# Kernel optimization log

Hardware: AMD Instinct MI355X
Metric: run time of the kernel (lower is better)

## Reference

```python
import jax, jax.numpy as jnp
import numpy as np

H = 64          # hiddens_dims
K = 3           # Chebyshev order
B = 16          # graphs in batch
NPG = 16384     # nodes per graph
N = B * NPG     # total nodes
E = 2_097_152   # total edges
R = 2191        # num_residues (hard-coded in source)
E_REF = R * 16
HALF = N // 2   # backbone count == sidechain count (mask is balanced per graph)


def _lin(k, fan_in, shape):
    return jax.random.uniform(k, shape, jnp.float32, -1.0, 1.0) / np.sqrt(fan_in)


def setup_inputs() -> dict:
    key = jax.random.key(0)
    ks = jax.random.split(key, 40)
    inp = {}
    inp["x"] = jax.random.normal(ks[0], (N, 3), jnp.float32)
    inp["edge_index"] = jax.random.randint(ks[1], (2, E), 0, N)
    inp["batch"] = jnp.repeat(jnp.arange(B, dtype=jnp.int32), NPG)
    blk = jnp.concatenate([jnp.ones((NPG // 2,), bool), jnp.zeros((NPG // 2,), bool)])
    inp["mask"] = jnp.tile(blk, B)  # backbone=True first half of each graph block
    inp["x_ref"] = jax.random.normal(ks[2], (R, 3), jnp.float32)
    inp["edgeref"] = jax.random.randint(ks[3], (2, E_REF), 0, R)
    i = 4
    for name, cin in [("cw0", 3), ("cw1", H), ("cw2", H), ("rw0", 3), ("rw1", H), ("rw2", H)]:
        inp[name] = _lin(ks[i], cin, (K, cin, H)); i += 1
        inp[name.replace("w", "b")] = jnp.zeros((H,), jnp.float32)  # ChebConv bias init = zeros
    for name, cin, cout in [("mlp_w", 2 * H, H), ("mlpP2_w", 2 * H, H),
                            ("rep0_w", H, H), ("rep1_w", H, H), ("rep2_w", H, 3)]:
        inp[name] = _lin(ks[i], cin, (cin, cout)); i += 1
        inp[name.replace("_w", "_b")] = _lin(ks[i], cin, (cout,)); i += 1
    return inp


def cheb_conv(x, edge_index, W, b, n):
    # PyG ChebConv with sym normalization, lambda_max=2: L_hat = -D^-1/2 A D^-1/2 (diag = 0)
    row, col = edge_index[0], edge_index[1]
    deg = jax.ops.segment_sum(jnp.ones_like(x[:, 0])[row] * 0 + 1.0, row, num_segments=n)
    dinv = jnp.where(deg > 0, jax.lax.rsqrt(jnp.maximum(deg, 1e-12)), 0.0)
    w = -(dinv[row] * dinv[col])  # [E]

    def prop(h):  # L_hat @ h via gather + segment_sum
        return jax.ops.segment_sum(w[:, None] * h[col], row, num_segments=n)

    Tx0 = x
    out = Tx0 @ W[0]
    Tx1 = prop(x)
    out = out + Tx1 @ W[1]
    for k in range(2, K):
        Tx2 = 2.0 * prop(Tx1) - Tx0
        out = out + Tx2 @ W[k]
        Tx0, Tx1 = Tx1, Tx2
    return out + b


def _forward(x, edge_index, mask, x_ref, edgeref,
             cw0, cb0, cw1, cb1, cw2, cb2, rw0, rb0, rw1, rb1, rw2, rb2,
             mlp_w, mlp_b, mlpP2_w, mlpP2_b,
             rep0_w, rep0_b, rep1_w, rep1_b, rep2_w, rep2_b):
    # main GNN stack (tanh after all but last; dropout is identity in eval)
    h = jnp.tanh(cheb_conv(x, edge_index, cw0, cb0, N))
    h = jnp.tanh(cheb_conv(h, edge_index, cw1, cb1, N))
    h = cheb_conv(h, edge_index, cw2, cb2, N)

    bb_idx = jnp.nonzero(mask, size=HALF)[0]
    sc_idx = jnp.nonzero(~mask, size=HALF)[0]
    x_bb = h[bb_idx].reshape(B, -1, H).mean(axis=1)[:, None, :]  # [B,1,H]
    x_sc = h[sc_idx].reshape(B, -1, H).mean(axis=1)[:, None, :]  # [B,1,H]

    # reference-graph stack: source bug makes `conv2 != self.convs[-1]` always True,
    # so tanh follows every convRef layer
    r = jnp.tanh(cheb_conv(x_ref, edgeref, rw0, rb0, R))
    r = jnp.tanh(cheb_conv(r, edgeref, rw1, rb1, R))
    r = jnp.tanh(cheb_conv(r, edgeref, rw2, rb2, R))
    r = jnp.broadcast_to(r[None], (B, R, H))

    bb_rep = jnp.broadcast_to(x_bb, (B, R, H))
    phase1 = jnp.concatenate([r, bb_rep], axis=-1) @ mlp_w + mlp_b        # [B,R,H]
    sc_rep = jnp.broadcast_to(x_sc, (B, R, H))
    phase2 = jnp.concatenate([phase1, sc_rep], axis=-1) @ mlpP2_w + mlpP2_b  # [B,R,H]

    res = phase2.reshape(-1, H)
    res = jax.nn.relu(res @ rep0_w + rep0_b)
    res = jax.nn.relu(res @ rep1_w + rep1_b)
    res = jax.nn.relu(res @ rep2_w + rep2_b)  # [B*R, 3]
    return res.reshape(-1, 3), x_bb, x_sc


def reference(x, edge_index, batch, mask, x_ref, edgeref,
              cw0, cb0, cw1, cb1, cw2, cb2, rw0, rb0, rw1, rb1, rw2, rb2,
              mlp_w, mlp_b, mlpP2_w, mlpP2_b,
              rep0_w, rep0_b, rep1_w, rep1_b, rep2_w, rep2_b):
    del batch  # only used for len(batch.unique()) == B, a static constant here
    return _forward(x, edge_index, mask, x_ref, edgeref,
                    cw0, cb0, cw1, cb1, cw2, cb2, rw0, rb0, rw1, rb1, rw2, rb2,
                    mlp_w, mlp_b, mlpP2_w, mlpP2_b,
                    rep0_w, rep0_b, rep1_w, rep1_b, rep2_w, rep2_b)
```

## Files before the change

kernel.cpp:

```cpp
#include <hip/hip_runtime.h>
#include <hip/hip_fp16.h>
#include <math.h>

#define NN 262144
#define NE 2097152
#define RR 2191
#define ER (RR*16)
#define NB 16
#define BRR (NB*RR)
#define OUT_RES (BRR*3)
#define NBKT 4096

typedef __attribute__((ext_vector_type(8))) _Float16 half8;
typedef __attribute__((ext_vector_type(4))) float f32x4;

__global__ void k_hist(const int* __restrict__ row, int* __restrict__ deg, int nE){
  int i = blockIdx.x*blockDim.x + threadIdx.x;
  int st = gridDim.x*blockDim.x;
  for (; i < nE; i += st) atomicAdd(&deg[row[i]], 1);
}

__global__ void k_scan1(const int* __restrict__ deg, int* __restrict__ rowptr,
                        int* __restrict__ partials, float* __restrict__ dinv){
  __shared__ int s[256];
  int t = threadIdx.x; int i = blockIdx.x*256 + t;
  int v = deg[i]; s[t] = v; __syncthreads();
  dinv[i] = v > 0 ? 1.0f/sqrtf((float)v) : 0.0f;
  for (int off = 1; off < 256; off <<= 1){
    int x = (t >= off) ? s[t-off] : 0; __syncthreads();
    s[t] += x; __syncthreads();
  }
  rowptr[i] = s[t] - v;
  if (t == 255) partials[blockIdx.x] = s[255];
}

__global__ void k_scan2(int* __restrict__ partials){
  __shared__ int s[1024];
  int t = threadIdx.x; int v = partials[t]; s[t] = v; __syncthreads();
  for (int off = 1; off < 1024; off <<= 1){
    int x = (t >= off) ? s[t-off] : 0; __syncthreads();
    s[t] += x; __syncthreads();
  }
  partials[t] = s[t] - v;
}

__global__ void k_scan3(int* __restrict__ rowptr, const int* __restrict__ partials){
  int t = threadIdx.x; int i = blockIdx.x*256 + t;
  rowptr[i] += partials[blockIdx.x];
  if (i == 0) rowptr[NN] = NE;
}

__global__ void k_scan_small(const int* __restrict__ deg, int* __restrict__ rowptr,
                             float* __restrict__ dinv, int n){
  __shared__ int s[256];
  int t = threadIdx.x;
  int carry = 0;
  for (int base = 0; base < n; base += 256){
    int idx = base + t;
    int v = (idx < n) ? deg[idx] : 0;
    if (idx < n) dinv[idx] = v > 0 ? 1.0f/sqrtf((float)v) : 0.0f;
    s[t] = v; __syncthreads();
    for (int off = 1; off < 256; off <<= 1){
      int x = (t >= off) ? s[t-off] : 0; __syncthreads();
      s[t] += x; __syncthreads();
    }
    if (idx < n) rowptr[idx] = carry + s[t] - v;
    carry += s[255];
    __syncthreads();
  }
  if (t == 0) rowptr[n] = carry;
}

__global__ void k_binA(const int* __restrict__ row, const int* __restrict__ col,
                       const float* __restrict__ dinv, const int* __restrict__ rowptr,
                       int* __restrict__ bcur, int2* __restrict__ staging, int nE){
  int i = blockIdx.x*blockDim.x + threadIdx.x;
  int st = gridDim.x*blockDim.x;
  for (; i < nE; i += st){
    int r = row[i], c = col[i];
    int b = r >> 6;
    int pos = rowptr[b << 6] + atomicAdd(&bcur[b], 1);
    float wv = -dinv[r]*dinv[c];
    staging[pos] = make_int2(((r & 63) << 24) | c, __float_as_int(wv));
  }
}

__global__ void __launch_bounds__(256) k_binB(const int2* __restrict__ staging,
                                              const int* __restrict__ rowptr,
                                              int2* __restrict__ cpair){
  __shared__ int rp[65];
  __shared__ int rowcur[64];
  int b = blockIdx.x;
  int t = threadIdx.x;
  if (t < 64){ rowcur[t] = 0; rp[t] = rowptr[(b << 6) + t]; }
  if (t == 64) rp[64] = rowptr[(b << 6) + 64];
  __syncthreads();
  int base = rp[0];
  int n_b = rp[64] - base;
  for (int i = t; i < n_b; i += 256){
    int2 pr = staging[base + i];
    int rl = (pr.x >> 24) & 63;
    int c  = pr.x & 0xFFFFFF;
    int idx = atomicAdd(&rowcur[rl], 1);
    cpair[rp[rl] + idx] = make_int2(c, pr.y);
  }
}

__global__ void k_scatter_ref(const int* __restrict__ row, const int* __restrict__ col,
                              const float* __restrict__ dinv, const int* __restrict__ rowptr,
                              int* __restrict__ cursor, int2* __restrict__ pair, int nE){
  int i = blockIdx.x*blockDim.x + threadIdx.x;
  int st = gridDim.x*blockDim.x;
  for (; i < nE; i += st){
    int r = row[i], c = col[i];
    int pos = rowptr[r] + atomicAdd(&cursor[r], 1);
    pair[pos] = make_int2(c, __float_as_int(-dinv[r]*dinv[c]));
  }
}

__global__ void k_prop3(const float* __restrict__ h, float* __restrict__ y,
                        const int* __restrict__ rowptr, const int2* __restrict__ pair, int n){
  int i = blockIdx.x*blockDim.x + threadIdx.x;
  if (i >= n) return;
  float a0 = 0.f, a1 = 0.f, a2 = 0.f;
  int s = rowptr[i], e = rowptr[i+1];
  int p = s;
  for (; p + 4 <= e; p += 4){
    int2 q0 = pair[p], q1 = pair[p+1], q2 = pair[p+2], q3 = pair[p+3];
    float w0 = __int_as_float(q0.y), w1 = __int_as_float(q1.y);
    float w2 = __int_as_float(q2.y), w3 = __int_as_float(q3.y);
    float x00=h[q0.x*3+0], x01=h[q0.x*3+1], x02=h[q0.x*3+2];
    float x10=h[q1.x*3+0], x11=h[q1.x*3+1], x12=h[q1.x*3+2];
    float x20=h[q2.x*3+0], x21=h[q2.x*3+1], x22=h[q2.x*3+2];
    float x30=h[q3.x*3+0], x31=h[q3.x*3+1], x32=h[q3.x*3+2];
    a0 = fmaf(w0,x00, fmaf(w1,x10, fmaf(w2,x20, fmaf(w3,x30, a0))));
    a1 = fmaf(w0,x01, fmaf(w1,x11, fmaf(w2,x21, fmaf(w3,x31, a1))));
    a2 = fmaf(w0,x02, fmaf(w1,x12, fmaf(w2,x22, fmaf(w3,x32, a2))));
  }
  for (; p < e; p++){
    int2 q = pair[p]; float wv = __int_as_float(q.y);
    a0 = fmaf(wv, h[q.x*3+0], a0); a1 = fmaf(wv, h[q.x*3+1], a1); a2 = fmaf(wv, h[q.x*3+2], a2);
  }
  y[i*3+0] = a0; y[i*3+1] = a1; y[i*3+2] = a2;
}

__global__ void k_prop64(const float* __restrict__ h, float* __restrict__ y,
                         const int* __restrict__ rowptr, const int2* __restrict__ pair, int n){
  int t = threadIdx.x, lane = t & 63;
  int i = blockIdx.x*4 + (t >> 6);
  if (i >= n) return;
  float acc = 0.f;
  int s = rowptr[i], e = rowptr[i+1];
  int p = s;
  for (; p + 4 <= e; p += 4){
    int2 q0 = pair[p], q1 = pair[p+1], q2 = pair[p+2], q3 = pair[p+3];
    float v0 = h[(size_t)q0.x*64 + lane], v1 = h[(size_t)q1.x*64 + lane];
    float v2 = h[(size_t)q2.x*64 + lane], v3 = h[(size_t)q3.x*64 + lane];
    acc = fmaf(__int_as_float(q0.y),v0, fmaf(__int_as_float(q1.y),v1,
          fmaf(__int_as_float(q2.y),v2, fmaf(__int_as_float(q3.y),v3, acc))));
  }
  for (; p < e; p++){
    int2 q = pair[p];
    acc = fmaf(__int_as_float(q.y), h[(size_t)q.x*64 + lane], acc);
  }
  y[(size_t)i*64 + lane] = acc;
}

__global__ void __launch_bounds__(256) k_prop64h(
    const uint2* __restrict__ h2, uint2* __restrict__ y2,
    const int* __restrict__ rowptr, const int2* __restrict__ pair, int n){
  int t = threadIdx.x;
  int sub = t & 15;
  int row = blockIdx.x*16 + (t >> 4);
  if (row >= n) return;
  int s = rowptr[row], e = rowptr[row+1];
  float a0=0.f, a1=0.f, a2=0.f, a3=0.f;
  int p = s;
  for (; p + 8 <= e; p += 8){
    int2 q[8]; uint2 v[8];
    #pragma unroll
    for (int j = 0; j < 8; j++) q[j] = pair[p+j];
    #pragma unroll
    for (int j = 0; j < 8; j++) v[j] = h2[(size_t)q[j].x*16 + sub];
    #pragma unroll
    for (int j = 0; j < 8; j++){
      float wv = __int_as_float(q[j].y);
      float2 fa = __half22float2(*(__half2*)&v[j].x);
      float2 fb = __half22float2(*(__half2*)&v[j].y);
      a0 = fmaf(wv, fa.x, a0); a1 = fmaf(wv, fa.y, a1);
      a2 = fmaf(wv, fb.x, a2); a3 = fmaf(wv, fb.y, a3);
    }
  }
  for (; p + 4 <= e; p += 4){
    int2 q[4]; uint2 v[4];
    #pragma unroll
    for (int j = 0; j < 4; j++) q[j] = pair[p+j];
    #pragma unroll
    for (int j = 0; j < 4; j++) v[j] = h2[(size_t)q[j].x*16 + sub];
    #pragma unroll
    for (int j = 0; j < 4; j++){
      float wv = __int_as_float(q[j].y);
      float2 fa = __half22float2(*(__half2*)&v[j].x);
      float2 fb = __half22float2(*(__half2*)&v[j].y);
      a0 = fmaf(wv, fa.x, a0); a1 = fmaf(wv, fa.y, a1);
      a2 = fmaf(wv, fb.x, a2); a3 = fmaf(wv, fb.y, a3);
    }
  }
  for (; p < e; p++){
    int2 q = pair[p];
    float wv = __int_as_float(q.y);
    uint2 v = h2[(size_t)q.x*16 + sub];
    float2 fa = __half22float2(*(__half2*)&v.x), fb = __half22float2(*(__half2*)&v.y);
    a0 = fmaf(wv, fa.x, a0); a1 = fmaf(wv, fa.y, a1);
    a2 = fmaf(wv, fb.x, a2); a3 = fmaf(wv, fb.y, a3);
  }
  __half2 lo = __floats2half2_rn(a0, a1), hi = __floats2half2_rn(a2, a3);
  uint2 r; r.x = *(unsigned*)&lo; r.y = *(unsigned*)&hi;
  y2[(size_t)row*16 + sub] = r;
}

__global__ void k_combine3f(const float* __restrict__ x, const float* __restrict__ t1,
                            const float* __restrict__ t2, const float* __restrict__ W,
                            const float* __restrict__ bias, float* __restrict__ out, int n){
  int t = threadIdx.x, lane = t & 63;
  int i = blockIdx.x*4 + (t >> 6);
  if (i >= n) return;
  float acc = bias[lane];
  #pragma unroll
  for (int j = 0; j < 3; j++){
    float x0 = x[i*3+j], x1 = t1[i*3+j];
    float x2 = 2.0f*t2[i*3+j] - x0;
    acc += x0*W[      j*64 + lane]
         + x1*W[192 + j*64 + lane]
         + x2*W[384 + j*64 + lane];
  }
  out[(size_t)i*64 + lane] = tanhf(acc);
}

__global__ void k_combine3h(const float* __restrict__ x, const float* __restrict__ t1,
                            const float* __restrict__ t2, const float* __restrict__ W,
                            const float* __restrict__ bias, __half* __restrict__ out, int n){
  int t = threadIdx.x, lane = t & 63;
  int i = blockIdx.x*4 + (t >> 6);
  if (i >= n) return;
  float acc = bias[lane];
  #pragma unroll
  for (int j = 0; j < 3; j++){
    float x0 = x[i*3+j], x1 = t1[i*3+j];
    float x2 = 2.0f*t2[i*3+j] - x0;
    acc += x0*W[      j*64 + lane]
         + x1*W[192 + j*64 + lane]
         + x2*W[384 + j*64 + lane];
  }
  out[(size_t)i*64 + lane] = __float2half_rn(tanhf(acc));
}

__global__ void k_weff(const float* __restrict__ W, float* __restrict__ D){
  int i = blockIdx.x*blockDim.x + threadIdx.x;
  D[i]        = W[i] - W[8192 + i];
  D[4096 + i] = W[4096 + i];
  D[8192 + i] = 2.0f * W[8192 + i];
}

__global__ void k_wpack(const float* __restrict__ W, _Float16* __restrict__ D){
  int t = blockIdx.x*blockDim.x + threadIdx.x;
  int reg = t & 7, lane = (t >> 3) & 63, nt = (t >> 9) & 3, kc = t >> 11;
  int m = kc >> 1;
  int kin = (kc & 1)*32 + ((lane >> 4) & 3)*8 + reg;
  int n = nt*16 + (lane & 15);
  float eff;
  if      (m == 0) eff = W[kin*64 + n] - W[8192 + kin*64 + n];
  else if (m == 1) eff = W[4096 + kin*64 + n];
  else             eff = 2.0f * W[8192 + kin*64 + n];
  D[t] = (_Float16)eff;
}

__global__ void __launch_bounds__(256) k_combine64m(
    const __half* A, const __half* B, const __half* C,
    const _Float16* __restrict__ wfrag, const float* __restrict__ bias,
    __half* out, int ntiles, int wavestride){
  int t = threadIdx.x;
  int lane = t & 63;
  int wv = blockIdx.x*4 + (t >> 6);
  half8 bf[24];
  #pragma unroll
  for (int i = 0; i < 24; i++)
    bf[i] = *(const half8*)(wfrag + ((size_t)(i*64 + lane))*8);
  int col = lane & 15, grp = (lane >> 4) & 3;
  float b0 = bias[col], b1 = bias[16+col], b2 = bias[32+col], b3 = bias[48+col];
  for (int tile = wv; tile < ntiles; tile += wavestride){
    size_t rb = (size_t)tile*16;
    f32x4 acc0 = {b0,b0,b0,b0}, acc1 = {b1,b1,b1,b1};
    f32x4 acc2 = {b2,b2,b2,b2}, acc3 = {b3,b3,b3,b3};
    #pragma unroll
    for (int kc = 0; kc < 6; kc++){
      const __half* s = (kc < 2) ? A : (kc < 4) ? B : C;
      half8 a = *(const half8*)(s + (rb + col)*64 + (kc & 1)*32 + grp*8);
      acc0 = __builtin_amdgcn_mfma_f32_16x16x32_f16(a, bf[kc*4+0], acc0, 0,0,0);
      acc1 = __builtin_amdgcn_mfma_f32_16x16x32_f16(a, bf[kc*4+1], acc1, 0,0,0);
      acc2 = __builtin_amdgcn_mfma_f32_16x16x32_f16(a, bf[kc*4+2], acc2, 0,0,0);
      acc3 = __builtin_amdgcn_mfma_f32_16x16x32_f16(a, bf[kc*4+3], acc3, 0,0,0);
    }
    __half* o = out + (rb + grp*4)*64;
    #pragma unroll
    for (int r = 0; r < 4; r++){
      o[(size_t)r*64 +      col] = __float2half_rn(tanhf(acc0[r]));
      o[(size_t)r*64 + 16 + col] = __float2half_rn(tanhf(acc1[r]));
      o[(size_t)r*64 + 32 + col] = __float2half_rn(tanhf(acc2[r]));
      o[(size_t)r*64 + 48 + col] = __float2half_rn(tanhf(acc3[r]));
    }
  }
}

__global__ void k_pool3(const __half2* __restrict__ hA, const __half2* __restrict__ hB,
                        const __half2* __restrict__ hC, float* __restrict__ pA,
                        float* __restrict__ pB, float* __restrict__ pC){
  const __half2* src = (blockIdx.y == 0) ? hA : (blockIdx.y == 1) ? hB : hC;
  float* dst         = (blockIdx.y == 0) ? pA : (blockIdx.y == 1) ? pB : pC;
  int blk = blockIdx.x;
  int chunk = blk & 15, seg = blk >> 4;
  int t = threadIdx.x, ch2 = t & 31, rsub = t >> 5;
  int base = seg*8192 + chunk*512;
  float ax = 0.f, ay = 0.f;
  for (int j = 0; j < 64; j++){
    int row = base + rsub + j*8;
    float2 v = __half22float2(src[(size_t)row*32 + ch2]);
    ax += v.x; ay += v.y;
  }
  __shared__ float sx[256], sy[256];
  sx[t] = ax; sy[t] = ay; __syncthreads();
  if (t < 32){
    float tx = 0.f, ty = 0.f;
    #pragma unroll
    for (int j = 0; j < 8; j++){ tx += sx[ch2 + j*32]; ty += sy[ch2 + j*32]; }
    int b = seg >> 1, half_ = seg & 1;
    atomicAdd(&dst[half_*1024 + b*64 + ch2*2],     tx);
    atomicAdd(&dst[half_*1024 + b*64 + ch2*2 + 1], ty);
  }
}

__global__ void k_combine_pooled(const float* __restrict__ pA, const float* __restrict__ pB,
                                 const float* __restrict__ pC, const float* __restrict__ weff,
                                 const float* __restrict__ bias, float* __restrict__ xbbsc,
                                 float* __restrict__ dout){
  int i = blockIdx.x*blockDim.x + threadIdx.x;
  int pr = i >> 6, c = i & 63;
  const float* a = pA + pr*64;
  const float* b = pB + pr*64;
  const float* cc = pC + pr*64;
  float v = 0.f;
  for (int k = 0; k < 64; k++){
    v = fmaf(a[k],  weff[        k*64 + c], v);
    v = fmaf(b[k],  weff[4096 +  k*64 + c], v);
    v = fmaf(cc[k], weff[8192 +  k*64 + c], v);
  }
  v = v*(1.0f/8192.0f) + bias[c];
  xbbsc[i] = v;
  dout[OUT_RES + i] = v;
}

__global__ void __launch_bounds__(256) k_combine64f(
    const float* __restrict__ A, const float* __restrict__ Bm, const float* __restrict__ C,
    const float* __restrict__ Weff, const float* __restrict__ bias,
    float* __restrict__ out, int n){
  int t = threadIdx.x;
  int lane = t & 63;
  int wid  = __builtin_amdgcn_readfirstlane(t >> 6);
  int half_ = wid & 1;
  int row  = blockIdx.x*128 + (wid >> 1)*64 + lane;
  bool active = (row < n);
  float acc[32];
  #pragma unroll
  for (int c = 0; c < 32; c++) acc[c] = bias[half_*32 + c];
  if (active){
    #pragma unroll 1
    for (int m = 0; m < 3; m++){
      const float* src = (m == 0 ? A : (m == 1 ? Bm : C)) + (size_t)row*64;
      const float* Wm  = Weff + m*4096 + half_*32;
      #pragma unroll 1
      for (int k4 = 0; k4 < 16; k4++){
        float4 a4 = *(const float4*)(src + k4*4);
        const float* wk = Wm + k4*256;
        #pragma unroll
        for (int kk = 0; kk < 4; kk++){
          float a = (kk == 0) ? a4.x : (kk == 1) ? a4.y : (kk == 2) ? a4.z : a4.w;
          #pragma unroll
          for (int c = 0; c < 32; c++)
            acc[c] = fmaf(a, wk[kk*64 + c], acc[c]);
        }
      }
    }
  }
  __syncthreads();
  if (active){
    float* o = out + (size_t)row*64 + half_*32;
    #pragma unroll
    for (int c = 0; c < 32; c++) o[c] = tanhf(acc[c]);
  }
}

__global__ void k_refchain(const float* __restrict__ refA, const float* __restrict__ mlp_w,
                           const float* __restrict__ mlp2_w, const float* __restrict__ rep0_w,
                           float* __restrict__ rt3a, int n){
  int t = threadIdx.x, lane = t & 63;
  int i = blockIdx.x*4 + (t >> 6);
  if (i >= n) return;
  float v = refA[i*64 + lane];
  float a = 0.f;
  #pragma unroll
  for (int k = 0; k < 64; k++) a += __shfl(v, k, 64) * mlp_w[k*64 + lane];
  float b = 0.f;
  #pragma unroll
  for (int k = 0; k < 64; k++) b += __shfl(a, k, 64) * mlp2_w[k*64 + lane];
  float c = 0.f;
  #pragma unroll
  for (int k = 0; k < 64; k++) c += __shfl(b, k, 64) * rep0_w[k*64 + lane];
  rt3a[i*64 + lane] = c;
}

__global__ void k_bbchain(const float* __restrict__ xbbsc,
                          const float* __restrict__ mlp_w,  const float* __restrict__ mlp_b,
                          const float* __restrict__ mlp2_w, const float* __restrict__ mlp2_b,
                          const float* __restrict__ rep0_w, const float* __restrict__ rep0_b,
                          float* __restrict__ bt3a){
  int t = threadIdx.x, lane = t & 63;
  int i = blockIdx.x*4 + (t >> 6);
  if (i >= NB) return;
  float vbb = xbbsc[i*64 + lane];
  float vsc = xbbsc[1024 + i*64 + lane];
  float a = mlp_b[lane];
  #pragma unroll
  for (int k = 0; k < 64; k++) a += __shfl(vbb, k, 64) * mlp_w[4096 + k*64 + lane];
  float b = mlp2_b[lane];
  #pragma unroll
  for (int k = 0; k < 64; k++) b += __shfl(a, k, 64) * mlp2_w[k*64 + lane];
  #pragma unroll
  for (int k = 0; k < 64; k++) b += __shfl(vsc, k, 64) * mlp2_w[4096 + k*64 + lane];
  float c = rep0_b[lane];
  #pragma unroll
  for (int k = 0; k < 64; k++) c += __shfl(b, k, 64) * rep0_w[k*64 + lane];
  bt3a[i*64 + lane] = c;
}

__global__ void k_final(const float* __restrict__ rt3, const float* __restrict__ bt3,
                        const float* __restrict__ W1, const float* __restrict__ b1,
                        const float* __restrict__ W2, const float* __restrict__ b2,
                        float* __restrict__ dout){
  int t = threadIdx.x, lane = t & 63;
  int g = blockIdx.x*4 + (t >> 6);
  if (g >= BRR) return;
  int b = g / RR, r = g - b*RR;
  float m = rt3[r*64 + lane] + bt3[b*64 + lane];
  m = fmaxf(m, 0.0f);
  float acc = b1[lane];
  #pragma unroll
  for (int k = 0; k < 64; k++) acc += __shfl(m, k, 64) * W1[k*64 + lane];
  float u = fmaxf(acc, 0.0f);
  float p0 = u*W2[lane*3+0], p1 = u*W2[lane*3+1], p2 = u*W2[lane*3+2];
  #pragma unroll
  for (int off = 32; off > 0; off >>= 1){
    p0 += __shfl_xor(p0, off, 64);
    p1 += __shfl_xor(p1, off, 64);
    p2 += __shfl_xor(p2, off, 64);
  }
  if (lane == 0){
    dout[g*3+0] = fmaxf(p0 + b2[0], 0.0f);
    dout[g*3+1] = fmaxf(p1 + b2[1], 0.0f);
    dout[g*3+2] = fmaxf(p2 + b2[2], 0.0f);
  }
}

extern "C" void kernel_launch(void* const* d_in, const int* in_sizes, int n_in,
                              void* d_out, int out_size, void* d_ws, size_t ws_size,
                              hipStream_t stream){
  const float* x     = (const float*)d_in[0];
  const int*   eidx  = (const int*)d_in[1];
  const float* x_ref = (const float*)d_in[4];
  const int*   eref  = (const int*)d_in[5];
  const float* cw0 = (const float*)d_in[6],  *cb0 = (const float*)d_in[7];
  const float* cw1 = (const float*)d_in[8],  *cb1 = (const float*)d_in[9];
  const float* cw2 = (const float*)d_in[10], *cb2 = (const float*)d_in[11];
  const float* rw0 = (const float*)d_in[12], *rb0 = (const float*)d_in[13];
  const float* rw1 = (const float*)d_in[14], *rb1 = (const float*)d_in[15];
  const float* rw2 = (const float*)d_in[16], *rb2 = (const float*)d_in[17];
  const float* mlp_w  = (const float*)d_in[18], *mlp_b  = (const float*)d_in[19];
  const float* mlp2_w = (const float*)d_in[20], *mlp2_b = (const float*)d_in[21];
  const float* rep0_w = (const float*)d_in[22], *rep0_b = (const float*)d_in[23];
  const float* rep1_w = (const float*)d_in[24], *rep1_b = (const float*)d_in[25];
  const float* rep2_w = (const float*)d_in[26], *rep2_b = (const float*)d_in[27];
  float* out = (float*)d_out;

  char* w = (char*)d_ws;
  size_t off = 0;
  auto alloc = [&](size_t bytes)->void*{
    void* p = w + off;
    off = (off + bytes + 255) & ~(size_t)255;
    return p;
  };
  int*   deg     = (int*)  alloc(NN*4);
  int*   bcur    = (int*)  alloc(NBKT*4);
  int*   degR    = (int*)  alloc(RR*4);
  int*   cursorR = (int*)  alloc(RR*4);
  float* poolA   = (float*)alloc(2048*4);
  float* poolB   = (float*)alloc(2048*4);
  float* poolC   = (float*)alloc(2048*4);
  size_t zero_bytes = off;

  int*   rowptr   = (int*)  alloc((NN+1)*4);
  int*   partials = (int*)  alloc(1024*4);
  int*   rowptrR  = (int*)  alloc((RR+1)*4);
  float* dinv     = (float*)alloc(NN*4);
  float* dinvR    = (float*)alloc(RR*4);
  int2*  staging  = (int2*) alloc((size_t)NE*8);
  int2*  cpair    = (int2*) alloc((size_t)NE*8);
  int2*  cpairR   = (int2*) alloc((size_t)ER*8);
  float* t1_3     = (float*)alloc((size_t)NN*3*4);
  float* t2_3     = (float*)alloc((size_t)NN*3*4);
  float* rt1_3    = (float*)alloc(RR*3*4);
  float* rt2_3    = (float*)alloc(RR*3*4);
  __half* hA      = (__half*)alloc((size_t)NN*64*2);
  __half* hB      = (__half*)alloc((size_t)NN*64*2);
  __half* hC      = (__half*)alloc((size_t)NN*64*2);
  float* refA     = (float*)alloc(RR*64*4);
  float* refB     = (float*)alloc(RR*64*4);
  float* refC     = (float*)alloc(RR*64*4);
  float* xbbsc    = (float*)alloc(2048*4);
  float* rt3a     = (float*)alloc(RR*64*4);
  float* bt3a     = (float*)alloc(NB*64*4);
  float* weffC2   = (float*)alloc(12288*4);
  float* weffR1   = (float*)alloc(12288*4);
  float* weffR2   = (float*)alloc(12288*4);
  _Float16* wfragC1 = (_Float16*)alloc(12288*2);
  (void)ws_size; (void)in_sizes; (void)n_in; (void)out_size;

  hipMemsetAsync(d_ws, 0, zero_bytes, stream);

  k_weff<<<16, 256, 0, stream>>>(cw2, weffC2);
  k_weff<<<16, 256, 0, stream>>>(rw1, weffR1);
  k_weff<<<16, 256, 0, stream>>>(rw2, weffR2);
  k_wpack<<<48, 256, 0, stream>>>(cw1, wfragC1);

  k_hist<<<2048, 256, 0, stream>>>(eidx, deg, NE);
  k_hist<<<64,   256, 0, stream>>>(eref, degR, ER);
  k_scan1<<<1024, 256, 0, stream>>>(deg, rowptr, partials, dinv);
  k_scan2<<<1, 1024, 0, stream>>>(partials);
  k_scan3<<<1024, 256, 0, stream>>>(rowptr, partials);
  k_scan_small<<<1, 256, 0, stream>>>(degR, rowptrR, dinvR, RR);
  k_binA<<<2048, 256, 0, stream>>>(eidx, eidx+NE, dinv, rowptr, bcur, staging, NE);
  k_binB<<<NBKT, 256, 0, stream>>>(staging, rowptr, cpair);
  k_scatter_ref<<<64, 256, 0, stream>>>(eref, eref+ER, dinvR, rowptrR, cursorR, cpairR, ER);

  k_prop3<<<1024, 256, 0, stream>>>(x, t1_3, rowptr, cpair, NN);
  k_prop3<<<1024, 256, 0, stream>>>(t1_3, t2_3, rowptr, cpair, NN);
  k_combine3h<<<NN/4, 256, 0, stream>>>(x, t1_3, t2_3, cw0, cb0, hA, NN);
  k_prop64h<<<NN/16, 256, 0, stream>>>((const uint2*)hA, (uint2*)hB, rowptr, cpair, NN);
  k_prop64h<<<NN/16, 256, 0, stream>>>((const uint2*)hB, (uint2*)hC, rowptr, cpair, NN);
  k_combine64m<<<1024, 256, 0, stream>>>(hA, hB, hC, wfragC1, cb1, hA, NN/16, 4096);
  k_prop64h<<<NN/16, 256, 0, stream>>>((const uint2*)hA, (uint2*)hB, rowptr, cpair, NN);
  k_prop64h<<<NN/16, 256, 0, stream>>>((const uint2*)hB, (uint2*)hC, rowptr, cpair, NN);
  k_pool3<<<dim3(512,3), 256, 0, stream>>>((const __half2*)hA, (const __half2*)hB,
                                           (const __half2*)hC, poolA, poolB, poolC);
  k_combine_pooled<<<8, 256, 0, stream>>>(poolA, poolB, poolC, weffC2, cb2, xbbsc, out);

  k_prop3<<<9, 256, 0, stream>>>(x_ref, rt1_3, rowptrR, cpairR, RR);
  k_prop3<<<9, 256, 0, stream>>>(rt1_3, rt2_3, rowptrR, cpairR, RR);
  k_combine3f<<<548, 256, 0, stream>>>(x_ref, rt1_3, rt2_3, rw0, rb0, refA, RR);
  k_prop64<<<548, 256, 0, stream>>>(refA, refB, rowptrR, cpairR, RR);
  k_prop64<<<548, 256, 0, stream>>>(refB, refC, rowptrR, cpairR, RR);
  k_combine64f<<<(RR+127)/128, 256, 0, stream>>>(refA, refB, refC, weffR1, rb1, refA, RR);
  k_prop64<<<548, 256, 0, stream>>>(refA, refB, rowptrR, cpairR, RR);
  k_prop64<<<548, 256, 0, stream>>>(refB, refC, rowptrR, cpairR, RR);
  k_combine64f<<<(RR+127)/128, 256, 0, stream>>>(refA, refB, refC, weffR2, rb2, refA, RR);

  k_refchain<<<548, 256, 0, stream>>>(refA, mlp_w, mlp2_w, rep0_w, rt3a, RR);
  k_bbchain<<<4, 256, 0, stream>>>(xbbsc, mlp_w, mlp_b, mlp2_w, mlp2_b, rep0_w, rep0_b, bt3a);

  k_final<<<(BRR+3)/4, 256, 0, stream>>>(rt3a, bt3a, rep1_w, rep1_b, rep2_w, rep2_b, out);
}
```

Measured before the change: 839.9 us.

## Pad 3-wide features to float4, widen fp16 gather, replace two-pass binning with direct scatter

The 3-channel node features are padded to float4 so each neighbour gather in the first Chebyshev propagations is one 16-byte load instead of three scalar loads. The 64-wide fp16 propagation now uses 8 lanes per row with 16-byte loads, giving 32 rows per block. The two-pass bucketed CSR build (binA staging plus binB local sort) is replaced by a single per-row atomic scatter, which drops the staging buffer but makes writes less local and adds more global atomics. Edge order within each row also becomes nondeterministic.

```diff
diff --git a/kernel.cpp b/kernel.cpp
--- a/kernel.cpp
+++ b/kernel.cpp
@@ -9,7 +9,6 @@
 #define NB 16
 #define BRR (NB*RR)
 #define OUT_RES (BRR*3)
-#define NBKT 4096
 
 typedef __attribute__((ext_vector_type(8))) _Float16 half8;
 typedef __attribute__((ext_vector_type(4))) float f32x4;
@@ -71,44 +70,9 @@
   if (t == 0) rowptr[n] = carry;
 }
 
-__global__ void k_binA(const int* __restrict__ row, const int* __restrict__ col,
-                       const float* __restrict__ dinv, const int* __restrict__ rowptr,
-                       int* __restrict__ bcur, int2* __restrict__ staging, int nE){
-  int i = blockIdx.x*blockDim.x + threadIdx.x;
-  int st = gridDim.x*blockDim.x;
-  for (; i < nE; i += st){
-    int r = row[i], c = col[i];
-    int b = r >> 6;
-    int pos = rowptr[b << 6] + atomicAdd(&bcur[b], 1);
-    float wv = -dinv[r]*dinv[c];
-    staging[pos] = make_int2(((r & 63) << 24) | c, __float_as_int(wv));
-  }
-}
-
-__global__ void __launch_bounds__(256) k_binB(const int2* __restrict__ staging,
-                                              const int* __restrict__ rowptr,
-                                              int2* __restrict__ cpair){
-  __shared__ int rp[65];
-  __shared__ int rowcur[64];
-  int b = blockIdx.x;
-  int t = threadIdx.x;
-  if (t < 64){ rowcur[t] = 0; rp[t] = rowptr[(b << 6) + t]; }
-  if (t == 64) rp[64] = rowptr[(b << 6) + 64];
-  __syncthreads();
-  int base = rp[0];
-  int n_b = rp[64] - base;
-  for (int i = t; i < n_b; i += 256){
-    int2 pr = staging[base + i];
-    int rl = (pr.x >> 24) & 63;
-    int c  = pr.x & 0xFFFFFF;
-    int idx = atomicAdd(&rowcur[rl], 1);
-    cpair[rp[rl] + idx] = make_int2(c, pr.y);
-  }
-}
-
-__global__ void k_scatter_ref(const int* __restrict__ row, const int* __restrict__ col,
-                              const float* __restrict__ dinv, const int* __restrict__ rowptr,
-                              int* __restrict__ cursor, int2* __restrict__ pair, int nE){
+__global__ void k_scatter(const int* __restrict__ row, const int* __restrict__ col,
+                          const float* __restrict__ dinv, const int* __restrict__ rowptr,
+                          int* __restrict__ cursor, int2* __restrict__ pair, int nE){
   int i = blockIdx.x*blockDim.x + threadIdx.x;
   int st = gridDim.x*blockDim.x;
   for (; i < nE; i += st){
@@ -118,8 +82,13 @@
   }
 }
 
-__global__ void k_prop3(const float* __restrict__ h, float* __restrict__ y,
-                        const int* __restrict__ rowptr, const int2* __restrict__ pair, int n){
+__global__ void k_pad3(const float* __restrict__ src, float4* __restrict__ dst, int n){
+  int i = blockIdx.x*blockDim.x + threadIdx.x;
+  if (i < n) dst[i] = make_float4(src[i*3], src[i*3+1], src[i*3+2], 0.0f);
+}
+
+__global__ void k_prop3p(const float4* __restrict__ h, float4* __restrict__ y,
+                         const int* __restrict__ rowptr, const int2* __restrict__ pair, int n){
   int i = blockIdx.x*blockDim.x + threadIdx.x;
   if (i >= n) return;
   float a0 = 0.f, a1 = 0.f, a2 = 0.f;
@@ -127,21 +96,19 @@
   int p = s;
   for (; p + 4 <= e; p += 4){
     int2 q0 = pair[p], q1 = pair[p+1], q2 = pair[p+2], q3 = pair[p+3];
+    float4 v0 = h[q0.x], v1 = h[q1.x], v2 = h[q2.x], v3 = h[q3.x];
     float w0 = __int_as_float(q0.y), w1 = __int_as_float(q1.y);
     float w2 = __int_as_float(q2.y), w3 = __int_as_float(q3.y);
-    float x00=h[q0.x*3+0], x01=h[q0.x*3+1], x02=h[q0.x*3+2];
-    float x10=h[q1.x*3+0], x11=h[q1.x*3+1], x12=h[q1.x*3+2];
-    float x20=h[q2.x*3+0], x21=h[q2.x*3+1], x22=h[q2.x*3+2];
-    float x30=h[q3.x*3+0], x31=h[q3.x*3+1], x32=h[q3.x*3+2];
-    a0 = fmaf(w0,x00, fmaf(w1,x10, fmaf(w2,x20, fmaf(w3,x30, a0))));
-    a1 = fmaf(w0,x01, fmaf(w1,x11, fmaf(w2,x21, fmaf(w3,x31, a1))));
-    a2 = fmaf(w0,x02, fmaf(w1,x12, fmaf(w2,x22, fmaf(w3,x32, a2))));
+    a0 = fmaf(w0,v0.x, fmaf(w1,v1.x, fmaf(w2,v2.x, fmaf(w3,v3.x, a0))));
+    a1 = fmaf(w0,v0.y, fmaf(w1,v1.y, fmaf(w2,v2.y, fmaf(w3,v3.y, a1))));
+    a2 = fmaf(w0,v0.z, fmaf(w1,v1.z, fmaf(w2,v2.z, fmaf(w3,v3.z, a2))));
   }
   for (; p < e; p++){
     int2 q = pair[p]; float wv = __int_as_float(q.y);
-    a0 = fmaf(wv, h[q.x*3+0], a0); a1 = fmaf(wv, h[q.x*3+1], a1); a2 = fmaf(wv, h[q.x*3+2], a2);
-  }
-  y[i*3+0] = a0; y[i*3+1] = a1; y[i*3+2] = a2;
+    float4 v = h[q.x];
+    a0 = fmaf(wv, v.x, a0); a1 = fmaf(wv, v.y, a1); a2 = fmaf(wv, v.z, a2);
+  }
+  y[i] = make_float4(a0, a1, a2, 0.0f);
 }
 
 __global__ void k_prop64(const float* __restrict__ h, float* __restrict__ y,
@@ -167,69 +134,86 @@
 }
 
 __global__ void __launch_bounds__(256) k_prop64h(
-    const uint2* __restrict__ h2, uint2* __restrict__ y2,
+    const uint4* __restrict__ h4, uint4* __restrict__ y4,
     const int* __restrict__ rowptr, const int2* __restrict__ pair, int n){
   int t = threadIdx.x;
-  int sub = t & 15;
-  int row = blockIdx.x*16 + (t >> 4);
+  int sub = t & 7;
+  int row = blockIdx.x*32 + (t >> 3);
   if (row >= n) return;
   int s = rowptr[row], e = rowptr[row+1];
-  float a0=0.f, a1=0.f, a2=0.f, a3=0.f;
+  float ac[8];
+  #pragma unroll
+  for (int k = 0; k < 8; k++) ac[k] = 0.f;
   int p = s;
   for (; p + 8 <= e; p += 8){
-    int2 q[8]; uint2 v[8];
+    int2 q[8]; uint4 v[8];
     #pragma unroll
     for (int j = 0; j < 8; j++) q[j] = pair[p+j];
     #pragma unroll
-    for (int j = 0; j < 8; j++) v[j] = h2[(size_t)q[j].x*16 + sub];
+    for (int j = 0; j < 8; j++) v[j] = h4[(size_t)q[j].x*8 + sub];
     #pragma unroll
     for (int j = 0; j < 8; j++){
       float wv = __int_as_float(q[j].y);
-      float2 fa = __half22float2(*(__half2*)&v[j].x);
-      float2 fb = __half22float2(*(__half2*)&v[j].y);
-      a0 = fmaf(wv, fa.x, a0); a1 = fmaf(wv, fa.y, a1);
-      a2 = fmaf(wv, fb.x, a2); a3 = fmaf(wv, fb.y, a3);
+      #pragma unroll
+      for (int k = 0; k < 4; k++){
+        float2 f = __half22float2(((const __half2*)&v[j])[k]);
+        ac[2*k]   = fmaf(wv, f.x, ac[2*k]);
+        ac[2*k+1] = fmaf(wv, f.y, ac[2*k+1]);
+      }
     }
   }
   for (; p + 4 <= e; p += 4){
-    int2 q[4]; uint2 v[4];
+    int2 q[4]; uint4 v[4];
     #pragma unroll
     for (int j = 0; j < 4; j++) q[j] = pair[p+j];
     #pragma unroll
-    for (int j = 0; j < 4; j++) v[j] = h2[(size_t)q[j].x*16 + sub];
+    for (int j = 0; j < 4; j++) v[j] = h4[(size_t)q[j].x*8 + sub];
     #pragma unroll
     for (int j = 0; j < 4; j++){
       float wv = __int_as_float(q[j].y);
-      float2 fa = __half22float2(*(__half2*)&v[j].x);
-      float2 fb = __half22float2(*(__half2*)&v[j].y);
-      a0 = fmaf(wv, fa.x, a0); a1 = fmaf(wv, fa.y, a1);
-      a2 = fmaf(wv, fb.x, a2); a3 = fmaf(wv, fb.y, a3);
+      #pragma unroll
+      for (int k = 0; k < 4; k++){
+        float2 f = __half22float2(((const __half2*)&v[j])[k]);
+        ac[2*k]   = fmaf(wv, f.x, ac[2*k]);
+        ac[2*k+1] = fmaf(wv, f.y, ac[2*k+1]);
+      }
     }
   }
   for (; p < e; p++){
     int2 q = pair[p];
     float wv = __int_as_float(q.y);
-    uint2 v = h2[(size_t)q.x*16 + sub];
-    float2 fa = __half22float2(*(__half2*)&v.x), fb = __half22float2(*(__half2*)&v.y);
-    a0 = fmaf(wv, fa.x, a0); a1 = fmaf(wv, fa.y, a1);
-    a2 = fmaf(wv, fb.x, a2); a3 = fmaf(wv, fb.y, a3);
-  }
-  __half2 lo = __floats2half2_rn(a0, a1), hi = __floats2half2_rn(a2, a3);
-  uint2 r; r.x = *(unsigned*)&lo; r.y = *(unsigned*)&hi;
-  y2[(size_t)row*16 + sub] = r;
-}
-
-__global__ void k_combine3f(const float* __restrict__ x, const float* __restrict__ t1,
-                            const float* __restrict__ t2, const float* __restrict__ W,
+    uint4 v = h4[(size_t)q.x*8 + sub];
+    #pragma unroll
+    for (int k = 0; k < 4; k++){
+      float2 f = __half22float2(((const __half2*)&v)[k]);
+      ac[2*k]   = fmaf(wv, f.x, ac[2*k]);
+      ac[2*k+1] = fmaf(wv, f.y, ac[2*k+1]);
+    }
+  }
+  uint4 r;
+  #pragma unroll
+  for (int k = 0; k < 4; k++){
+    __half2 hp = __floats2half2_rn(ac[2*k], ac[2*k+1]);
+    ((unsigned*)&r)[k] = *(unsigned*)&hp;
+  }
+  y4[(size_t)row*8 + sub] = r;
+}
+
+__global__ void k_combine3f(const float4* __restrict__ x, const float4* __restrict__ t1,
+                            const float4* __restrict__ t2, const float* __restrict__ W,
                             const float* __restrict__ bias, float* __restrict__ out, int n){
   int t = threadIdx.x, lane = t & 63;
   int i = blockIdx.x*4 + (t >> 6);
   if (i >= n) return;
+  float4 px = x[i], p1 = t1[i], p2 = t2[i];
+  const float* fx = (const float*)&px;
+  const float* f1 = (const float*)&p1;
+  const float* f2 = (const float*)&p2;
   float acc = bias[lane];
   #pragma unroll
   for (int j = 0; j < 3; j++){
-    float x0 = x[i*3+j], x1 = t1[i*3+j];
-    float x2 = 2.0f*t2[i*3+j] - x0;
+    float x0 = fx[j], x1 = f1[j];
+    float x2 = 2.0f*f2[j] - x0;
     acc += x0*W[      j*64 + lane]
          + x1*W[192 + j*64 + lane]
          + x2*W[384 + j*64 + lane];
@@ -237,17 +221,21 @@
   out[(size_t)i*64 + lane] = tanhf(acc);
 }
 
-__global__ void k_combine3h(const float* __restrict__ x, const float* __restrict__ t1,
-                            const float* __restrict__ t2, const float* __restrict__ W,
+__global__ void k_combine3h(const float4* __restrict__ x, const float4* __restrict__ t1,
+                            const float4* __restrict__ t2, const float* __restrict__ W,
                             const float* __restrict__ bias, __half* __restrict__ out, int n){
   int t = threadIdx.x, lane = t & 63;
   int i = blockIdx.x*4 + (t >> 6);
   if (i >= n) return;
+  float4 px = x[i], p1 = t1[i], p2 = t2[i];
+  const float* fx = (const float*)&px;
+  const float* f1 = (const float*)&p1;
+  const float* f2 = (const float*)&p2;
   float acc = bias[lane];
   #pragma unroll
   for (int j = 0; j < 3; j++){
-    float x0 = x[i*3+j], x1 = t1[i*3+j];
-    float x2 = 2.0f*t2[i*3+j] - x0;
+    float x0 = fx[j], x1 = f1[j];
+    float x2 = 2.0f*f2[j] - x0;
     acc += x0*W[      j*64 + lane]
          + x1*W[192 + j*64 + lane]
          + x2*W[384 + j*64 + lane];
@@ -498,7 +486,7 @@
     return p;
   };
   int*   deg     = (int*)  alloc(NN*4);
-  int*   bcur    = (int*)  alloc(NBKT*4);
+  int*   cursor  = (int*)  alloc(NN*4);
   int*   degR    = (int*)  alloc(RR*4);
   int*   cursorR = (int*)  alloc(RR*4);
   float* poolA   = (float*)alloc(2048*4);
@@ -511,13 +499,14 @@
   int*   rowptrR  = (int*)  alloc((RR+1)*4);
   float* dinv     = (float*)alloc(NN*4);
   float* dinvR    = (float*)alloc(RR*4);
-  int2*  staging  = (int2*) alloc((size_t)NE*8);
   int2*  cpair    = (int2*) alloc((size_t)NE*8);
   int2*  cpairR   = (int2*) alloc((size_t)ER*8);
-  float* t1_3     = (float*)alloc((size_t)NN*3*4);
-  float* t2_3     = (float*)alloc((size_t)NN*3*4);
-  float* rt1_3    = (float*)alloc(RR*3*4);
-  float* rt2_3    = (float*)alloc(RR*3*4);
+  float4* x4      = (float4*)alloc((size_t)NN*16);
+  float4* t1_4    = (float4*)alloc((size_t)NN*16);
+  float4* t2_4    = (float4*)alloc((size_t)NN*16);
+  float4* xr4     = (float4*)alloc((size_t)RR*16);
+  float4* rt1_4   = (float4*)alloc((size_t)RR*16);
+  float4* rt2_4   = (float4*)alloc((size_t)RR*16);
   __half* hA      = (__half*)alloc((size_t)NN*64*2);
   __half* hB      = (__half*)alloc((size_t)NN*64*2);
   __half* hC      = (__half*)alloc((size_t)NN*64*2);
@@ -539,6 +528,8 @@
   k_weff<<<16, 256, 0, stream>>>(rw1, weffR1);
   k_weff<<<16, 256, 0, stream>>>(rw2, weffR2);
   k_wpack<<<48, 256, 0, stream>>>(cw1, wfragC1);
+  k_pad3<<<1024, 256, 0, stream>>>(x, x4, NN);
+  k_pad3<<<9, 256, 0, stream>>>(x_ref, xr4, RR);
 
   k_hist<<<2048, 256, 0, stream>>>(eidx, deg, NE);
   k_hist<<<64,   256, 0, stream>>>(eref, degR, ER);
@@ -546,25 +537,24 @@
   k_scan2<<<1, 1024, 0, stream>>>(partials);
   k_scan3<<<1024, 256, 0, stream>>>(rowptr, partials);
   k_scan_small<<<1, 256, 0, stream>>>(degR, rowptrR, dinvR, RR);
-  k_binA<<<2048, 256, 0, stream>>>(eidx, eidx+NE, dinv, rowptr, bcur, staging, NE);
-  k_binB<<<NBKT, 256, 0, stream>>>(staging, rowptr, cpair);
-  k_scatter_ref<<<64, 256, 0, stream>>>(eref, eref+ER, dinvR, rowptrR, cursorR, cpairR, ER);
-
-  k_prop3<<<1024, 256, 0, stream>>>(x, t1_3, rowptr, cpair, NN);
-  k_prop3<<<1024, 256, 0, stream>>>(t1_3, t2_3, rowptr, cpair, NN);
-  k_combine3h<<<NN/4, 256, 0, stream>>>(x, t1_3, t2_3, cw0, cb0, hA, NN);
-  k_prop64h<<<NN/16, 256, 0, stream>>>((const uint2*)hA, (uint2*)hB, rowptr, cpair, NN);
-  k_prop64h<<<NN/16, 256, 0, stream>>>((const uint2*)hB, (uint2*)hC, rowptr, cpair, NN);
+  k_scatter<<<2048, 256, 0, stream>>>(eidx, eidx+NE, dinv, rowptr, cursor, cpair, NE);
+  k_scatter<<<64,   256, 0, stream>>>(eref, eref+ER, dinvR, rowptrR, cursorR, cpairR, ER);
+
+  k_prop3p<<<1024, 256, 0, stream>>>(x4, t1_4, rowptr, cpair, NN);
+  k_prop3p<<<1024, 256, 0, stream>>>(t1_4, t2_4, rowptr, cpair, NN);
+  k_combine3h<<<NN/4, 256, 0, stream>>>(x4, t1_4, t2_4, cw0, cb0, hA, NN);
+  k_prop64h<<<NN/32, 256, 0, stream>>>((const uint4*)hA, (uint4*)hB, rowptr, cpair, NN);
+  k_prop64h<<<NN/32, 256, 0, stream>>>((const uint4*)hB, (uint4*)hC, rowptr, cpair, NN);
   k_combine64m<<<1024, 256, 0, stream>>>(hA, hB, hC, wfragC1, cb1, hA, NN/16, 4096);
-  k_prop64h<<<NN/16, 256, 0, stream>>>((const uint2*)hA, (uint2*)hB, rowptr, cpair, NN);
-  k_prop64h<<<NN/16, 256, 0, stream>>>((const uint2*)hB, (uint2*)hC, rowptr, cpair, NN);
+  k_prop64h<<<NN/32, 256, 0, stream>>>((const uint4*)hA, (uint4*)hB, rowptr, cpair, NN);
+  k_prop64h<<<NN/32, 256, 0, stream>>>((const uint4*)hB, (uint4*)hC, rowptr, cpair, NN);
   k_pool3<<<dim3(512,3), 256, 0, stream>>>((const __half2*)hA, (const __half2*)hB,
                                            (const __half2*)hC, poolA, poolB, poolC);
   k_combine_pooled<<<8, 256, 0, stream>>>(poolA, poolB, poolC, weffC2, cb2, xbbsc, out);
 
-  k_prop3<<<9, 256, 0, stream>>>(x_ref, rt1_3, rowptrR, cpairR, RR);
-  k_prop3<<<9, 256, 0, stream>>>(rt1_3, rt2_3, rowptrR, cpairR, RR);
-  k_combine3f<<<548, 256, 0, stream>>>(x_ref, rt1_3, rt2_3, rw0, rb0, refA, RR);
+  k_prop3p<<<9, 256, 0, stream>>>(xr4, rt1_4, rowptrR, cpairR, RR);
+  k_prop3p<<<9, 256, 0, stream>>>(rt1_4, rt2_4, rowptrR, cpairR, RR);
+  k_combine3f<<<548, 256, 0, stream>>>(xr4, rt1_4, rt2_4, rw0, rb0, refA, RR);
   k_prop64<<<548, 256, 0, stream>>>(refA, refB, rowptrR, cpairR, RR);
   k_prop64<<<548, 256, 0, stream>>>(refB, refC, rowptrR, cpairR, RR);
   k_combine64f<<<(RR+127)/128, 256, 0, stream>>>(refA, refB, refC, weffR1, rb1, refA, RR);
```

Result: faster. 769.9 us (-8.3%).
